# Kernel tuning notes

Measured on AMD Instinct MI355X. Metric: run time of the kernel, lower is better.

Reference implementation:

```python
import jax, jax.numpy as jnp
import numpy as np

C = 256
HEAD_DIM = 8
N_HEAD = C // HEAD_DIM  # 32
GN_GROUPS = max(1, C // 32)  # 8
GN_EPS = 1e-5


def setup_inputs() -> dict:
    key = jax.random.key(0)
    ks = jax.random.split(key, 7)
    x = jax.random.normal(ks[0], (8, C, 32, 32), dtype=jnp.float32)
    gn_w = jax.random.normal(ks[1], (C,), dtype=jnp.float32) * 0.02 + 1.0
    gn_b = jax.random.normal(ks[2], (C,), dtype=jnp.float32) * 0.02
    qkv_w = jax.random.normal(ks[3], (3 * C, C), dtype=jnp.float32) / np.sqrt(C)
    qkv_b = jax.random.normal(ks[4], (3 * C,), dtype=jnp.float32) * 0.01
    out_w = jax.random.normal(ks[5], (C, C), dtype=jnp.float32) / np.sqrt(C)
    out_b = jax.random.normal(ks[6], (C,), dtype=jnp.float32) * 0.01
    return {"x": x, "gn_w": gn_w, "gn_b": gn_b, "qkv_w": qkv_w,
            "qkv_b": qkv_b, "out_w": out_w, "out_b": out_b}


def reference(x, gn_w, gn_b, qkv_w, qkv_b, out_w, out_b):
    n, c, h, w = x.shape
    hw = h * w
    # --- GroupNorm ---
    xg = x.reshape(n, GN_GROUPS, c // GN_GROUPS * hw)
    mu = jnp.mean(xg, axis=-1, keepdims=True)
    var = jnp.var(xg, axis=-1, keepdims=True)
    xn = ((xg - mu) * jax.lax.rsqrt(var + GN_EPS)).reshape(n, c, hw)
    xn = xn * gn_w[None, :, None] + gn_b[None, :, None]
    # --- QKV 1x1 conv ---
    qkv = jnp.einsum('oc,nct->not', qkv_w, xn) + qkv_b[None, :, None]  # [n,3c,hw]
    qkv = qkv.reshape(n, 3, N_HEAD, HEAD_DIM, hw)
    q, k, v = qkv[:, 0], qkv[:, 1], qkv[:, 2]  # each [n, heads, hd, hw]
    # --- attention over hw tokens ---
    scale = 1.0 / np.sqrt(HEAD_DIM)
    att = jnp.einsum('nhds,nhdt->nhst', q, k) * scale  # [n,heads,hw,hw]
    att = jax.nn.softmax(att, axis=-1)
    y = jnp.einsum('nhst,nhdt->nhds', att, v)  # [n,heads,hd,hw]
    y = y.reshape(n, c, hw)
    # --- output 1x1 conv + residual ---
    out = jnp.einsum('oc,nct->not', out_w, y) + out_b[None, :, None]
    return x + out.reshape(n, c, h, w)
```

## Files before the change

kernel.cpp:

```cpp
#include <hip/hip_runtime.h>
#include <hip/hip_bf16.h>
#include <math.h>


#define NBATCH 8
#define C 256
#define HW 1024
#define NHEAD 32
#define HDIM 8

typedef __bf16 bf16x8 __attribute__((ext_vector_type(8)));
typedef __bf16 bf16x4 __attribute__((ext_vector_type(4)));
typedef _Float16 f16x8 __attribute__((ext_vector_type(8)));
typedef _Float16 f16x4 __attribute__((ext_vector_type(4)));
typedef float floatx4 __attribute__((ext_vector_type(4)));
typedef float floatx16 __attribute__((ext_vector_type(16)));

#if __has_builtin(__builtin_amdgcn_exp2f)
#define EXP2F(x) __builtin_amdgcn_exp2f(x)
#else
#define EXP2F(x) exp2f(x)
#endif

#define SCALE_LOG2E 0.51013249662f

__global__ __launch_bounds__(256) void cvt_kernel(
    const float* __restrict__ qw, const float* __restrict__ ow,
    __bf16* __restrict__ wq, __bf16* __restrict__ wo)
{
    int id = blockIdx.x * 256 + threadIdx.x;
    float4 v;
    __bf16* dst;
    if (id < 49152) { v = *(const float4*)&qw[id * 4]; dst = wq + id * 4; }
    else { v = *(const float4*)&ow[(id - 49152) * 4]; dst = wo + (id - 49152) * 4; }
    bf16x4 o = { (__bf16)v.x, (__bf16)v.y, (__bf16)v.z, (__bf16)v.w };
    *(bf16x4*)dst = o;
}

__global__ __launch_bounds__(256) void gn_stats_kernel(
    const float* __restrict__ x, float* __restrict__ stats)
{
    int blk = blockIdx.x;
    int part = blk & 7, ng = blk >> 3;
    const float4* xv = (const float4*)(x + ((size_t)ng * 32 + part * 4) * HW);
    int tid = threadIdx.x;
    float s = 0.f, ss = 0.f;
#pragma unroll
    for (int i = 0; i < 4; ++i) {
        float4 v = xv[tid + i * 256];
        s  += v.x + v.y + v.z + v.w;
        ss += v.x*v.x + v.y*v.y + v.z*v.z + v.w*v.w;
    }
#pragma unroll
    for (int o = 32; o; o >>= 1) { s += __shfl_xor(s, o); ss += __shfl_xor(ss, o); }
    __shared__ float rs[4], rss[4];
    int wave = tid >> 6, lane = tid & 63;
    if (lane == 0) { rs[wave] = s; rss[wave] = ss; }
    __syncthreads();
    if (tid == 0) {
        stats[blk * 2]     = rs[0] + rs[1] + rs[2] + rs[3];
        stats[blk * 2 + 1] = rss[0] + rss[1] + rss[2] + rss[3];
    }
}

__global__ __launch_bounds__(256) void gn_apply_kernel(
    const float* __restrict__ x, const float* __restrict__ w,
    const float* __restrict__ b, const float* __restrict__ stats,
    __bf16* __restrict__ xnT)
{
    int blk = blockIdx.x;
    int chunk = blk & 3, ng = blk >> 2;
    int n = ng >> 3, g = ng & 7;
    float s = 0.f, ss = 0.f;
#pragma unroll
    for (int p = 0; p < 8; ++p) {
        s  += stats[(ng * 8 + p) * 2];
        ss += stats[(ng * 8 + p) * 2 + 1];
    }
    const float invN = 1.0f / 32768.0f;
    float mean = s * invN;
    float var  = ss * invN - mean * mean;
    float rstd = rsqrtf(var + 1e-5f);
    const float* xp = x + ((size_t)ng * 32) * HW;
    int tid = threadIdx.x, t0 = chunk * 256;
    __shared__ __bf16 Lt[32][257];
#pragma unroll 8
    for (int c = 0; c < 32; ++c) {
        float wc = w[g * 32 + c] * rstd;
        float bc = b[g * 32 + c] - mean * wc;
        float v = xp[(size_t)c * HW + t0 + tid];
        Lt[c][tid] = (__bf16)(v * wc + bc);
    }
    __syncthreads();
    __bf16* xo = xnT + (size_t)n * HW * C + g * 32;
#pragma unroll
    for (int q = 0; q < 4; ++q) {
        bf16x8 o;
#pragma unroll
        for (int e = 0; e < 8; ++e) o[e] = Lt[q * 8 + e][tid];
        *(bf16x8*)&xo[(size_t)(t0 + tid) * C + q * 8] = o;
    }
}

__global__ __launch_bounds__(256) void gemm_qkv_kernel(
    const __bf16* __restrict__ W, const __bf16* __restrict__ Ball,
    const float* __restrict__ bias, _Float16* __restrict__ Qf,
    _Float16* __restrict__ Kf, __bf16* __restrict__ Vbf)
{
    int n = blockIdx.z;
    const __bf16* B = Ball + (size_t)n * HW * C;
    int om0 = blockIdx.y * 64, t0 = blockIdx.x * 128;
    __shared__ __bf16 As[64 * 32];
    __shared__ __bf16 Bs[128 * 32];
    int tid = threadIdx.x, lane = tid & 63, wave = tid >> 6;
    int l15 = lane & 15, quad = lane >> 4;
    int wm = (wave & 1) * 32, wn = (wave >> 1) * 64;
    int swq = (quad ^ (l15 & 3)) * 8;
    int arow = tid >> 2, aq = tid & 3;
    int sw = (aq ^ (arow & 3)) * 8;
    floatx4 acc[2][4] = {};
    for (int c0 = 0; c0 < C; c0 += 32) {
        bf16x8 av  = *(const bf16x8*)&W[(size_t)(om0 + arow) * C + c0 + aq * 8];
        bf16x8 bv0 = *(const bf16x8*)&B[(size_t)(t0 + arow) * C + c0 + aq * 8];
        bf16x8 bv1 = *(const bf16x8*)&B[(size_t)(t0 + 64 + arow) * C + c0 + aq * 8];
        __syncthreads();
        *(bf16x8*)&As[arow * 32 + sw] = av;
        *(bf16x8*)&Bs[arow * 32 + sw] = bv0;
        *(bf16x8*)&Bs[(arow + 64) * 32 + sw] = bv1;
        __syncthreads();
        bf16x8 af[2], bfr[4];
#pragma unroll
        for (int mi = 0; mi < 2; ++mi)
            af[mi] = *(const bf16x8*)&As[(wm + mi * 16 + l15) * 32 + swq];
#pragma unroll
        for (int ni = 0; ni < 4; ++ni)
            bfr[ni] = *(const bf16x8*)&Bs[(wn + ni * 16 + l15) * 32 + swq];
#pragma unroll
        for (int mi = 0; mi < 2; ++mi)
#pragma unroll
            for (int ni = 0; ni < 4; ++ni)
                acc[mi][ni] = __builtin_amdgcn_mfma_f32_16x16x32_bf16(
                    af[mi], bfr[ni], acc[mi][ni], 0, 0, 0);
    }
#pragma unroll
    for (int mi = 0; mi < 2; ++mi) {
        int obase = om0 + wm + mi * 16;
        int oq = obase + quad * 4;
        if (obase < 512) {
            int h  = (oq & 255) >> 3;
            int d0 = (quad & 1) * 4;
            _Float16* dst = (obase < 256 ? Qf : Kf);
            float mul = (obase < 256) ? SCALE_LOG2E : 1.0f;
#pragma unroll
            for (int ni = 0; ni < 4; ++ni) {
                int t = t0 + wn + ni * 16 + l15;
                f16x4 o;
#pragma unroll
                for (int r = 0; r < 4; ++r)
                    o[r] = (_Float16)((acc[mi][ni][r] + bias[oq + r]) * mul);
                *(f16x4*)&dst[(((size_t)(n * 32 + h)) * HW + t) * 8 + d0] = o;
            }
        } else {
            int cv = oq - 512;
#pragma unroll
            for (int ni = 0; ni < 4; ++ni) {
                int t = t0 + wn + ni * 16 + l15;
#pragma unroll
                for (int r = 0; r < 4; ++r)
                    Vbf[((size_t)(n * 256 + cv + r)) * HW + t] =
                        (__bf16)(acc[mi][ni][r] + bias[oq + r]);
            }
        }
    }
}

__global__ __launch_bounds__(256) void gemm_out_kernel(
    const __bf16* __restrict__ W, const __bf16* __restrict__ Ball,
    const float* __restrict__ bias, float* __restrict__ Call,
    const float* __restrict__ Rall)
{
    int n = blockIdx.z;
    const __bf16* B = Ball + (size_t)n * HW * C;
    float* Cp = Call + (size_t)n * C * HW;
    const float* R = Rall + (size_t)n * C * HW;
    int om0 = blockIdx.y * 64, t0 = blockIdx.x * 64;
    __shared__ __bf16 As[64 * 32];
    __shared__ __bf16 Bs[64 * 32];
    int tid = threadIdx.x, lane = tid & 63, wave = tid >> 6;
    int l15 = lane & 15, quad = lane >> 4;
    int wm = (wave & 1) * 32, wn = (wave >> 1) * 32;
    int swq = (quad ^ (l15 & 3)) * 8;
    int arow = tid >> 2, aq = tid & 3;
    int sw = (aq ^ (arow & 3)) * 8;
    floatx4 acc[2][2] = {};
    for (int c0 = 0; c0 < C; c0 += 32) {
        bf16x8 av = *(const bf16x8*)&W[(size_t)(om0 + arow) * C + c0 + aq * 8];
        bf16x8 bv = *(const bf16x8*)&B[(size_t)(t0 + arow) * C + c0 + aq * 8];
        __syncthreads();
        *(bf16x8*)&As[arow * 32 + sw] = av;
        *(bf16x8*)&Bs[arow * 32 + sw] = bv;
        __syncthreads();
        bf16x8 af[2], bfr[2];
#pragma unroll
        for (int mi = 0; mi < 2; ++mi)
            af[mi] = *(const bf16x8*)&As[(wm + mi * 16 + l15) * 32 + swq];
#pragma unroll
        for (int ni = 0; ni < 2; ++ni)
            bfr[ni] = *(const bf16x8*)&Bs[(wn + ni * 16 + l15) * 32 + swq];
#pragma unroll
        for (int mi = 0; mi < 2; ++mi)
#pragma unroll
            for (int ni = 0; ni < 2; ++ni)
                acc[mi][ni] = __builtin_amdgcn_mfma_f32_16x16x32_bf16(
                    af[mi], bfr[ni], acc[mi][ni], 0, 0, 0);
    }
#pragma unroll
    for (int mi = 0; mi < 2; ++mi) {
#pragma unroll
        for (int r = 0; r < 4; ++r) {
            int o = om0 + wm + mi * 16 + quad * 4 + r;
            float bb = bias[o];
#pragma unroll
            for (int ni = 0; ni < 2; ++ni) {
                int t = t0 + wn + ni * 16 + l15;
                Cp[(size_t)o * HW + t] = acc[mi][ni][r] + bb + R[(size_t)o * HW + t];
            }
        }
    }
}

__global__ __launch_bounds__(256, 4) void attn_kernel(
    const _Float16* __restrict__ Qf, const _Float16* __restrict__ Kf,
    const __bf16* __restrict__ Vg, __bf16* __restrict__ yT)
{
    int quarter = blockIdx.x & 3, h = (blockIdx.x >> 2) & 31, n = blockIdx.x >> 7;
    __shared__ alignas(16) _Float16 Kb[HW][8];
    __shared__ alignas(16) __bf16   Vb[9][HW + 8];
    int tid = threadIdx.x;
    const _Float16* kg = Kf + ((size_t)(n * 32 + h)) * HW * 8;
    const __bf16*   vg = Vg + ((size_t)(n * 256 + h * 8)) * HW;
#pragma unroll
    for (int i = 0; i < 4; ++i) {
        int row = tid + i * 256;
        *(f16x8*)&Kb[row][0] = *(const f16x8*)&kg[(size_t)row * 8];
    }
#pragma unroll
    for (int i = 0; i < 4; ++i) {
        int id = tid + i * 256;
        int d = id >> 7, t8 = (id & 127) * 8;
        *(bf16x8*)&Vb[d][t8] = *(const bf16x8*)&vg[(size_t)d * HW + t8];
    }
    if (tid < 128) {
        __bf16 one = (__bf16)1.0f;
        bf16x8 ones = { one, one, one, one, one, one, one, one };
        *(bf16x8*)&Vb[8][tid * 8] = ones;
    }
    int lane = tid & 63, wave = tid >> 6;
    int l31 = lane & 31, lhi = lane >> 5;
    int vrow = l31 < 9 ? l31 : (l31 & 7);
    const __bf16* vbase = &Vb[vrow][0];
    int tqb = quarter * 256 + wave * 64;
    const _Float16* qg = Qf + ((size_t)(n * 32 + h)) * HW * 8;
    f16x8 qf[2];
#pragma unroll
    for (int tau = 0; tau < 2; ++tau) {
        f16x8 qv = { 0, 0, 0, 0, 0, 0, 0, 0 };
        if (lhi == 0)
            qv = *(const f16x8*)&qg[(size_t)(tqb + tau * 32 + l31) * 8];
        qf[tau] = qv;
    }
    __syncthreads();
    floatx16 accG[2] = {};
    floatx16 zero16 = {};
    for (int tkt = 0; tkt < 32; ++tkt) {
        f16x8 kf = *(const f16x8*)&Kb[tkt * 32 + l31][0];
        int cb = tkt * 32 + lhi * 4;
        bf16x4 va0 = *(const bf16x4*)&vbase[cb];
        bf16x4 va1 = *(const bf16x4*)&vbase[cb + 8];
        bf16x4 va2 = *(const bf16x4*)&vbase[cb + 16];
        bf16x4 va3 = *(const bf16x4*)&vbase[cb + 24];
        bf16x8 vf0 = __builtin_shufflevector(va0, va1, 0, 1, 2, 3, 4, 5, 6, 7);
        bf16x8 vf1 = __builtin_shufflevector(va2, va3, 0, 1, 2, 3, 4, 5, 6, 7);
#pragma unroll
        for (int tau = 0; tau < 2; ++tau) {
            floatx16 sT = __builtin_amdgcn_mfma_f32_32x32x16_f16(
                kf, qf[tau], zero16, 0, 0, 0);
            __bf16 p[16];
#pragma unroll
            for (int r = 0; r < 16; ++r) p[r] = (__bf16)EXP2F(sT[r]);
            bf16x8 P0 = { p[0], p[1], p[2], p[3], p[4], p[5], p[6], p[7] };
            bf16x8 P1 = { p[8], p[9], p[10], p[11], p[12], p[13], p[14], p[15] };
            accG[tau] = __builtin_amdgcn_mfma_f32_32x32x16_bf16(
                vf0, P0, accG[tau], 0, 0, 0);
            accG[tau] = __builtin_amdgcn_mfma_f32_32x32x16_bf16(
                vf1, P1, accG[tau], 0, 0, 0);
        }
    }
    __bf16* yp = yT + (size_t)n * HW * C + h * HDIM + lhi * 4;
#pragma unroll
    for (int tau = 0; tau < 2; ++tau) {
        float own4 = accG[tau][4];
        float part4 = __shfl_xor(own4, 32);
        float lsum = lhi ? part4 : own4;
        float inv = 1.0f / lsum;
        bf16x4 o = { (__bf16)(accG[tau][0] * inv), (__bf16)(accG[tau][1] * inv),
                     (__bf16)(accG[tau][2] * inv), (__bf16)(accG[tau][3] * inv) };
        *(bf16x4*)&yp[(size_t)(tqb + tau * 32 + l31) * C] = o;
    }
}

extern "C" void kernel_launch(void* const* d_in, const int* in_sizes, int n_in,
                              void* d_out, int out_size, void* d_ws, size_t ws_size,
                              hipStream_t stream)
{
    const float* x     = (const float*)d_in[0];
    const float* gn_w  = (const float*)d_in[1];
    const float* gn_b  = (const float*)d_in[2];
    const float* qkv_w = (const float*)d_in[3];
    const float* qkv_b = (const float*)d_in[4];
    const float* out_w = (const float*)d_in[5];
    const float* out_b = (const float*)d_in[6];
    float* out = (float*)d_out;

    char* wsb = (char*)d_ws;
    __bf16*   xnT = (__bf16*)wsb;
    _Float16* Qf  = (_Float16*)(wsb + ((size_t)4 << 20));
    _Float16* Kf  = (_Float16*)(wsb + ((size_t)8 << 20));
    __bf16*   Vbf = (__bf16*)(wsb + ((size_t)12 << 20));
    __bf16*   yTp = (__bf16*)(wsb + ((size_t)16 << 20));
    __bf16*   wq  = (__bf16*)(wsb + ((size_t)20 << 20));
    __bf16*   wo  = wq + (size_t)3 * C * C;
    float*    st  = (float*)(wsb + ((size_t)21 << 20));

    cvt_kernel<<<256, 256, 0, stream>>>(qkv_w, out_w, wq, wo);
    gn_stats_kernel<<<512, 256, 0, stream>>>(x, st);
    gn_apply_kernel<<<256, 256, 0, stream>>>(x, gn_w, gn_b, st, xnT);
    gemm_qkv_kernel<<<dim3(8, 12, 8), 256, 0, stream>>>(wq, xnT, qkv_b,
                                                        Qf, Kf, Vbf);
    attn_kernel<<<1024, 256, 0, stream>>>(Qf, Kf, Vbf, yTp);
    gemm_out_kernel<<<dim3(16, 4, 8), 256, 0, stream>>>(wo, yTp, out_b, out, x);
}
```

Baseline: 127.0 us.

## Fuse weight conversion into GN stats and double-buffer B tiles in GEMMs

Merges the weight bf16 conversion kernel into the GroupNorm stats kernel to save one launch. Both GEMM kernels now read the weight (A) fragments directly from global memory into registers instead of staging them through LDS. The B tile is double-buffered in LDS, with the next tile prefetched during the MFMAs, which leaves one barrier per k-step instead of two. This trades LDS traffic and barriers for uncoalesced direct global A loads, which lean on cache reuse.

```diff
diff --git a/kernel.cpp b/kernel.cpp
--- a/kernel.cpp
+++ b/kernel.cpp
@@ -24,26 +24,25 @@
 
 #define SCALE_LOG2E 0.51013249662f
 
-__global__ __launch_bounds__(256) void cvt_kernel(
+__global__ __launch_bounds__(256) void gn_stats_cvt_kernel(
+    const float* __restrict__ x, float* __restrict__ stats,
     const float* __restrict__ qw, const float* __restrict__ ow,
     __bf16* __restrict__ wq, __bf16* __restrict__ wo)
 {
-    int id = blockIdx.x * 256 + threadIdx.x;
-    float4 v;
-    __bf16* dst;
-    if (id < 49152) { v = *(const float4*)&qw[id * 4]; dst = wq + id * 4; }
-    else { v = *(const float4*)&ow[(id - 49152) * 4]; dst = wo + (id - 49152) * 4; }
-    bf16x4 o = { (__bf16)v.x, (__bf16)v.y, (__bf16)v.z, (__bf16)v.w };
-    *(bf16x4*)dst = o;
-}
-
-__global__ __launch_bounds__(256) void gn_stats_kernel(
-    const float* __restrict__ x, float* __restrict__ stats)
-{
     int blk = blockIdx.x;
+    int tid = threadIdx.x;
+    if (blk >= 512) {
+        int id = (blk - 512) * 256 + tid;
+        float4 v;
+        __bf16* dst;
+        if (id < 49152) { v = *(const float4*)&qw[id * 4]; dst = wq + id * 4; }
+        else { v = *(const float4*)&ow[(id - 49152) * 4]; dst = wo + (id - 49152) * 4; }
+        bf16x4 o = { (__bf16)v.x, (__bf16)v.y, (__bf16)v.z, (__bf16)v.w };
+        *(bf16x4*)dst = o;
+        return;
+    }
     int part = blk & 7, ng = blk >> 3;
     const float4* xv = (const float4*)(x + ((size_t)ng * 32 + part * 4) * HW);
-    int tid = threadIdx.x;
     float s = 0.f, ss = 0.f;
 #pragma unroll
     for (int i = 0; i < 4; ++i) {
@@ -110,37 +109,49 @@
     int n = blockIdx.z;
     const __bf16* B = Ball + (size_t)n * HW * C;
     int om0 = blockIdx.y * 64, t0 = blockIdx.x * 128;
-    __shared__ __bf16 As[64 * 32];
-    __shared__ __bf16 Bs[128 * 32];
+    __shared__ __bf16 Bs[2][128 * 32];
     int tid = threadIdx.x, lane = tid & 63, wave = tid >> 6;
     int l15 = lane & 15, quad = lane >> 4;
     int wm = (wave & 1) * 32, wn = (wave >> 1) * 64;
     int swq = (quad ^ (l15 & 3)) * 8;
+    int brow = tid >> 1, bq = tid & 1;
     int arow = tid >> 2, aq = tid & 3;
     int sw = (aq ^ (arow & 3)) * 8;
+    const __bf16* a0 = &W[(size_t)(om0 + wm + l15) * C + quad * 8];
+    const __bf16* a1 = &W[(size_t)(om0 + wm + 16 + l15) * C + quad * 8];
     floatx4 acc[2][4] = {};
-    for (int c0 = 0; c0 < C; c0 += 32) {
-        bf16x8 av  = *(const bf16x8*)&W[(size_t)(om0 + arow) * C + c0 + aq * 8];
-        bf16x8 bv0 = *(const bf16x8*)&B[(size_t)(t0 + arow) * C + c0 + aq * 8];
-        bf16x8 bv1 = *(const bf16x8*)&B[(size_t)(t0 + 64 + arow) * C + c0 + aq * 8];
+    {
+        bf16x8 bv0 = *(const bf16x8*)&B[(size_t)(t0 + arow) * C + aq * 8];
+        bf16x8 bv1 = *(const bf16x8*)&B[(size_t)(t0 + 64 + arow) * C + aq * 8];
+        *(bf16x8*)&Bs[0][arow * 32 + sw] = bv0;
+        *(bf16x8*)&Bs[0][(arow + 64) * 32 + sw] = bv1;
         __syncthreads();
-        *(bf16x8*)&As[arow * 32 + sw] = av;
-        *(bf16x8*)&Bs[arow * 32 + sw] = bv0;
-        *(bf16x8*)&Bs[(arow + 64) * 32 + sw] = bv1;
-        __syncthreads();
+    }
+#pragma unroll
+    for (int k = 0; k < 8; ++k) {
+        int c0 = k * 32;
+        bf16x8 bv0, bv1;
+        if (k < 7) {
+            bv0 = *(const bf16x8*)&B[(size_t)(t0 + arow) * C + c0 + 32 + aq * 8];
+            bv1 = *(const bf16x8*)&B[(size_t)(t0 + 64 + arow) * C + c0 + 32 + aq * 8];
+        }
         bf16x8 af[2], bfr[4];
-#pragma unroll
-        for (int mi = 0; mi < 2; ++mi)
-            af[mi] = *(const bf16x8*)&As[(wm + mi * 16 + l15) * 32 + swq];
+        af[0] = *(const bf16x8*)&a0[c0];
+        af[1] = *(const bf16x8*)&a1[c0];
 #pragma unroll
         for (int ni = 0; ni < 4; ++ni)
-            bfr[ni] = *(const bf16x8*)&Bs[(wn + ni * 16 + l15) * 32 + swq];
+            bfr[ni] = *(const bf16x8*)&Bs[k & 1][(wn + ni * 16 + l15) * 32 + swq];
 #pragma unroll
         for (int mi = 0; mi < 2; ++mi)
 #pragma unroll
             for (int ni = 0; ni < 4; ++ni)
                 acc[mi][ni] = __builtin_amdgcn_mfma_f32_16x16x32_bf16(
                     af[mi], bfr[ni], acc[mi][ni], 0, 0, 0);
+        if (k < 7) {
+            *(bf16x8*)&Bs[(k + 1) & 1][arow * 32 + sw] = bv0;
+            *(bf16x8*)&Bs[(k + 1) & 1][(arow + 64) * 32 + sw] = bv1;
+            __syncthreads();
+        }
     }
 #pragma unroll
     for (int mi = 0; mi < 2; ++mi) {
@@ -184,35 +195,43 @@
     float* Cp = Call + (size_t)n * C * HW;
     const float* R = Rall + (size_t)n * C * HW;
     int om0 = blockIdx.y * 64, t0 = blockIdx.x * 64;
-    __shared__ __bf16 As[64 * 32];
-    __shared__ __bf16 Bs[64 * 32];
+    __shared__ __bf16 Bs[2][64 * 32];
     int tid = threadIdx.x, lane = tid & 63, wave = tid >> 6;
     int l15 = lane & 15, quad = lane >> 4;
     int wm = (wave & 1) * 32, wn = (wave >> 1) * 32;
     int swq = (quad ^ (l15 & 3)) * 8;
     int arow = tid >> 2, aq = tid & 3;
     int sw = (aq ^ (arow & 3)) * 8;
+    const __bf16* a0 = &W[(size_t)(om0 + wm + l15) * C + quad * 8];
+    const __bf16* a1 = &W[(size_t)(om0 + wm + 16 + l15) * C + quad * 8];
     floatx4 acc[2][2] = {};
-    for (int c0 = 0; c0 < C; c0 += 32) {
-        bf16x8 av = *(const bf16x8*)&W[(size_t)(om0 + arow) * C + c0 + aq * 8];
-        bf16x8 bv = *(const bf16x8*)&B[(size_t)(t0 + arow) * C + c0 + aq * 8];
+    {
+        bf16x8 bv = *(const bf16x8*)&B[(size_t)(t0 + arow) * C + aq * 8];
+        *(bf16x8*)&Bs[0][arow * 32 + sw] = bv;
         __syncthreads();
-        *(bf16x8*)&As[arow * 32 + sw] = av;
-        *(bf16x8*)&Bs[arow * 32 + sw] = bv;
-        __syncthreads();
+    }
+#pragma unroll
+    for (int k = 0; k < 8; ++k) {
+        int c0 = k * 32;
+        bf16x8 bv;
+        if (k < 7)
+            bv = *(const bf16x8*)&B[(size_t)(t0 + arow) * C + c0 + 32 + aq * 8];
         bf16x8 af[2], bfr[2];
-#pragma unroll
-        for (int mi = 0; mi < 2; ++mi)
-            af[mi] = *(const bf16x8*)&As[(wm + mi * 16 + l15) * 32 + swq];
+        af[0] = *(const bf16x8*)&a0[c0];
+        af[1] = *(const bf16x8*)&a1[c0];
 #pragma unroll
         for (int ni = 0; ni < 2; ++ni)
-            bfr[ni] = *(const bf16x8*)&Bs[(wn + ni * 16 + l15) * 32 + swq];
+            bfr[ni] = *(const bf16x8*)&Bs[k & 1][(wn + ni * 16 + l15) * 32 + swq];
 #pragma unroll
         for (int mi = 0; mi < 2; ++mi)
 #pragma unroll
             for (int ni = 0; ni < 2; ++ni)
                 acc[mi][ni] = __builtin_amdgcn_mfma_f32_16x16x32_bf16(
                     af[mi], bfr[ni], acc[mi][ni], 0, 0, 0);
+        if (k < 7) {
+            *(bf16x8*)&Bs[(k + 1) & 1][arow * 32 + sw] = bv;
+            __syncthreads();
+        }
     }
 #pragma unroll
     for (int mi = 0; mi < 2; ++mi) {
@@ -332,8 +351,7 @@
     __bf16*   wo  = wq + (size_t)3 * C * C;
     float*    st  = (float*)(wsb + ((size_t)21 << 20));
 
-    cvt_kernel<<<256, 256, 0, stream>>>(qkv_w, out_w, wq, wo);
-    gn_stats_kernel<<<512, 256, 0, stream>>>(x, st);
+    gn_stats_cvt_kernel<<<768, 256, 0, stream>>>(x, st, qkv_w, out_w, wq, wo);
     gn_apply_kernel<<<256, 256, 0, stream>>>(x, gn_w, gn_b, st, xnT);
     gemm_qkv_kernel<<<dim3(8, 12, 8), 256, 0, stream>>>(wq, xnT, qkv_b,
                                                         Qf, Kf, Vbf);
```

After: 131.0 us. +3.1%, slower.
